# Performance work log

Measured on AMD Instinct MI355X. Metric: run time of the kernel, lower is better.

Reference implementation:

```python
import jax, jax.numpy as jnp
import numpy as np
import math

B, DG, P, DA = 512, 1024, 1024, 256
LN_EPS = 1e-5  # torch LayerNorm default
EPS = 1e-12


def _ln(x, g, b):
    mu = jnp.mean(x, axis=-1, keepdims=True)
    var = jnp.mean((x - mu) ** 2, axis=-1, keepdims=True)
    return (x - mu) * jax.lax.rsqrt(var + LN_EPS) * g + b


def setup_inputs() -> dict:
    key = jax.random.key(0)
    ks = jax.random.split(key, 16)
    s = lambda fan_in: 1.0 / math.sqrt(fan_in)
    return {
        "hg": jax.random.normal(ks[0], (B, DG), jnp.float32),
        "desc_2d": jax.random.normal(ks[1], (B, P), jnp.float32),
        "Wq": jax.random.uniform(ks[2], (DA, DG), jnp.float32, -s(DG), s(DG)),
        "bq": jnp.zeros((DA,), jnp.float32),
        "wk_val": jax.random.uniform(ks[3], (DA,), jnp.float32, -1.0, 1.0),
        "bk_val": jax.random.uniform(ks[4], (DA,), jnp.float32, -1.0, 1.0),
        "wv_val": jax.random.uniform(ks[5], (DA,), jnp.float32, -1.0, 1.0),
        "bv_val": jax.random.uniform(ks[6], (DA,), jnp.float32, -1.0, 1.0),
        "Ek": jax.random.normal(ks[7], (P, DA), jnp.float32),
        "Ev": jax.random.normal(ks[8], (P, DA), jnp.float32),
        "Uq": jax.random.uniform(ks[9], (DA, DA), jnp.float32, -s(DA), s(DA)),
        "Vk": jax.random.uniform(ks[10], (DA, DA), jnp.float32, -s(DA), s(DA)),
        "ln_q_g": jnp.ones((DA,), jnp.float32), "ln_q_b": jnp.zeros((DA,), jnp.float32),
        "ln_k_g": jnp.ones((DA,), jnp.float32), "ln_k_b": jnp.zeros((DA,), jnp.float32),
        "ln_v_g": jnp.ones((DA,), jnp.float32), "ln_v_b": jnp.zeros((DA,), jnp.float32),
    }


def reference(hg, desc_2d, Wq, bq, wk_val, bk_val, wv_val, bv_val, Ek, Ev, Uq, Vk,
              ln_q_g, ln_q_b, ln_k_g, ln_k_b, ln_v_g, ln_v_b):
    # dropout is inference-mode (identity)
    q = _ln(hg @ Wq.T + bq, ln_q_g, ln_q_b)                       # (B, DA)
    # scalar -> token proj plus id embedding
    k = desc_2d[:, :, None] * wk_val + bk_val + Ek[None]          # (B, P, DA)
    v = desc_2d[:, :, None] * wv_val + bv_val + Ev[None]
    k = _ln(k, ln_k_g, ln_k_b)
    v = _ln(v, ln_v_g, ln_v_b)
    q2 = q @ Uq.T                                                 # (B, DA)
    k2 = jnp.einsum('bpd,ed->bpe', k, Vk)                         # (B, P, DA)
    e = jnp.einsum('bpd,bd->bp', k2, q2) / math.sqrt(DA)          # (B, P)
    alpha = jax.nn.sigmoid(e)
    alpha = alpha / (jnp.sum(alpha, axis=1, keepdims=True) + EPS)
    c = jnp.einsum('bp,bpd->bd', alpha, v)                        # (B, DA)
    return c, alpha
```

## Files before the change

### kernel.cpp

```cpp
#include <hip/hip_runtime.h>
#include <math.h>

#define B 512
#define DG 1024
#define P 1024
#define DA 256
#define LDP 68

__device__ __forceinline__ float block_reduce_sum(float v, volatile float* red) {
    #pragma unroll
    for (int off = 32; off > 0; off >>= 1) v += __shfl_down(v, off, 64);
    const int lane = threadIdx.x & 63, wid = threadIdx.x >> 6;
    __syncthreads();
    if (lane == 0) red[wid] = v;
    __syncthreads();
    return red[0] + red[1] + red[2] + red[3];
}

#define FMA16(a4, b4, acc)                                   \
    acc[0][0] = fmaf(a4.x, b4.x, acc[0][0]);                 \
    acc[0][1] = fmaf(a4.x, b4.y, acc[0][1]);                 \
    acc[0][2] = fmaf(a4.x, b4.z, acc[0][2]);                 \
    acc[0][3] = fmaf(a4.x, b4.w, acc[0][3]);                 \
    acc[1][0] = fmaf(a4.y, b4.x, acc[1][0]);                 \
    acc[1][1] = fmaf(a4.y, b4.y, acc[1][1]);                 \
    acc[1][2] = fmaf(a4.y, b4.z, acc[1][2]);                 \
    acc[1][3] = fmaf(a4.y, b4.w, acc[1][3]);                 \
    acc[2][0] = fmaf(a4.z, b4.x, acc[2][0]);                 \
    acc[2][1] = fmaf(a4.z, b4.y, acc[2][1]);                 \
    acc[2][2] = fmaf(a4.z, b4.z, acc[2][2]);                 \
    acc[2][3] = fmaf(a4.z, b4.w, acc[2][3]);                 \
    acc[3][0] = fmaf(a4.w, b4.x, acc[3][0]);                 \
    acc[3][1] = fmaf(a4.w, b4.y, acc[3][1]);                 \
    acc[3][2] = fmaf(a4.w, b4.z, acc[3][2]);                 \
    acc[3][3] = fmaf(a4.w, b4.w, acc[3][3]);

#define FMA8(a0, a1, b4, acc)                                \
    acc[0][0] = fmaf(a0, b4.x, acc[0][0]);                   \
    acc[0][1] = fmaf(a0, b4.y, acc[0][1]);                   \
    acc[0][2] = fmaf(a0, b4.z, acc[0][2]);                   \
    acc[0][3] = fmaf(a0, b4.w, acc[0][3]);                   \
    acc[1][0] = fmaf(a1, b4.x, acc[1][0]);                   \
    acc[1][1] = fmaf(a1, b4.y, acc[1][1]);                   \
    acc[1][2] = fmaf(a1, b4.z, acc[1][2]);                   \
    acc[1][3] = fmaf(a1, b4.w, acc[1][3]);

__global__ __launch_bounds__(256) void KA(const float* __restrict__ hg, const float* __restrict__ Wq,
                                          const float* __restrict__ Uq, const float* __restrict__ Vk,
                                          const float* __restrict__ Ek, const float* __restrict__ Ev,
                                          const float* __restrict__ wk, const float* __restrict__ bk,
                                          const float* __restrict__ wv, const float* __restrict__ bv,
                                          const float* __restrict__ gk, const float* __restrict__ bkln,
                                          float* __restrict__ qp, float* __restrict__ Gm,
                                          float* __restrict__ pst, float* __restrict__ scal4,
                                          float* __restrict__ vec4) {
    __shared__ __align__(16) float sA[32 * LDP];
    __shared__ __align__(16) float sB[32 * LDP];
    __shared__ float red[4];
    const int tid = threadIdx.x;
    const int bi = blockIdx.x;

    if (bi < 256) {
        const int mt = bi & 7, nt = (bi >> 3) & 3, ks = bi >> 5;
        const int b0 = mt * 64, d0 = nt * 64, kc = ks * 128;
        const int sm = tid >> 3, sk4 = (tid & 7) * 4;
        const int ty4 = (tid >> 4) * 4, tx4 = (tid & 15) * 4;
        float acc[4][4] = {};
        for (int kt = 0; kt < 128; kt += 32) {
            const int kg = kc + kt;
            #pragma unroll
            for (int pass = 0; pass < 2; ++pass) {
                int m = sm + pass * 32;
                float4 av = *reinterpret_cast<const float4*>(&hg[(b0 + m) * DG + kg + sk4]);
                sA[(sk4 + 0) * LDP + m] = av.x; sA[(sk4 + 1) * LDP + m] = av.y;
                sA[(sk4 + 2) * LDP + m] = av.z; sA[(sk4 + 3) * LDP + m] = av.w;
                float4 wv4 = *reinterpret_cast<const float4*>(&Wq[(d0 + m) * DG + kg + sk4]);
                sB[(sk4 + 0) * LDP + m] = wv4.x; sB[(sk4 + 1) * LDP + m] = wv4.y;
                sB[(sk4 + 2) * LDP + m] = wv4.z; sB[(sk4 + 3) * LDP + m] = wv4.w;
            }
            __syncthreads();
            #pragma unroll
            for (int kk = 0; kk < 32; ++kk) {
                float4 a4 = *reinterpret_cast<const float4*>(&sA[kk * LDP + ty4]);
                float4 b4 = *reinterpret_cast<const float4*>(&sB[kk * LDP + tx4]);
                FMA16(a4, b4, acc)
            }
            __syncthreads();
        }
        float* outp = qp + ks * (B * DA);
        #pragma unroll
        for (int i = 0; i < 4; ++i) {
            float4 o = make_float4(acc[i][0], acc[i][1], acc[i][2], acc[i][3]);
            *reinterpret_cast<float4*>(&outp[(b0 + ty4 + i) * DA + d0 + tx4]) = o;
        }
    } else if (bi < 384) {
        const int b2 = bi - 256;
        const int e0 = (b2 & 7) * 32, p0 = (b2 >> 3) * 64;
        const int sm = tid >> 3, sk4 = (tid & 7) * 4;
        const int ty = tid >> 4, tx4 = (tid & 15) * 4;
        float acc[2][4] = {};
        for (int kt = 0; kt < 256; kt += 32) {
            float4 vv = *reinterpret_cast<const float4*>(&Vk[(e0 + sm) * DA + kt + sk4]);
            float4 gg = *reinterpret_cast<const float4*>(&gk[kt + sk4]);
            sA[(sk4 + 0) * LDP + sm] = vv.x * gg.x; sA[(sk4 + 1) * LDP + sm] = vv.y * gg.y;
            sA[(sk4 + 2) * LDP + sm] = vv.z * gg.z; sA[(sk4 + 3) * LDP + sm] = vv.w * gg.w;
            #pragma unroll
            for (int pass = 0; pass < 2; ++pass) {
                int m = sm + pass * 32;
                float4 ee = *reinterpret_cast<const float4*>(&Ek[(p0 + m) * DA + kt + sk4]);
                sB[(sk4 + 0) * LDP + m] = ee.x; sB[(sk4 + 1) * LDP + m] = ee.y;
                sB[(sk4 + 2) * LDP + m] = ee.z; sB[(sk4 + 3) * LDP + m] = ee.w;
            }
            __syncthreads();
            #pragma unroll
            for (int kk = 0; kk < 32; ++kk) {
                float a0 = sA[kk * LDP + ty * 2 + 0];
                float a1 = sA[kk * LDP + ty * 2 + 1];
                float4 b4 = *reinterpret_cast<const float4*>(&sB[kk * LDP + tx4]);
                FMA8(a0, a1, b4, acc)
            }
            __syncthreads();
        }
        #pragma unroll
        for (int i = 0; i < 2; ++i) {
            float4 o = make_float4(acc[i][0], acc[i][1], acc[i][2], acc[i][3]);
            *reinterpret_cast<float4*>(&Gm[(e0 + ty * 2 + i) * P + p0 + tx4]) = o;
        }
    } else if (bi == 384) {
        float* w4  = sA;
        float* tmp = sB;
        float gkd = gk[tid];
        w4[0 * 256 + tid] = wk[tid] * gkd;
        w4[1 * 256 + tid] = bk[tid] * gkd;
        w4[2 * 256 + tid] = gkd;
        w4[3 * 256 + tid] = bkln[tid];
        __syncthreads();
        const int dl = tid & 15, eg = tid >> 4;
        for (int eb = 0; eb < 16; ++eb) {
            int e = eb * 16 + eg;
            float p0 = 0.f, p1 = 0.f, p2 = 0.f, p3 = 0.f;
            #pragma unroll
            for (int t = 0; t < 16; ++t) {
                int d = dl + t * 16;
                float v = Vk[e * DA + d];
                p0 = fmaf(v, w4[d], p0);
                p1 = fmaf(v, w4[256 + d], p1);
                p2 = fmaf(v, w4[512 + d], p2);
                p3 = fmaf(v, w4[768 + d], p3);
            }
            #pragma unroll
            for (int m = 8; m > 0; m >>= 1) {
                p0 += __shfl_xor(p0, m, 16);
                p1 += __shfl_xor(p1, m, 16);
                p2 += __shfl_xor(p2, m, 16);
                p3 += __shfl_xor(p3, m, 16);
            }
            if (dl == 0) {
                tmp[e * 4 + 0] = p0; tmp[e * 4 + 1] = p1;
                tmp[e * 4 + 2] = p2; tmp[e * 4 + 3] = p3;
            }
        }
        __syncthreads();
        float a0 = 0.f, a1 = 0.f, a2 = 0.f, a3 = 0.f;
        for (int e = 0; e < 256; ++e) {
            float u = Uq[e * DA + tid];
            a0 = fmaf(u, tmp[e * 4 + 0], a0);
            a1 = fmaf(u, tmp[e * 4 + 1], a1);
            a2 = fmaf(u, tmp[e * 4 + 2], a2);
            a3 = fmaf(u, tmp[e * 4 + 3], a3);
        }
        vec4[tid] = a0; vec4[256 + tid] = a1; vec4[512 + tid] = a2; vec4[768 + tid] = a3;
    } else {
        const int p = bi - 385, d = tid;
        const float inv = 1.0f / DA;
        float ek = Ek[p * DA + d], ev = Ev[p * DA + d];
        float wkd = wk[d], wvd = wv[d];
        float ck = bk[d] + ek, cv = bv[d] + ev;

        float Sck  = block_reduce_sum(ck, red);
        float Sck2 = block_reduce_sum(ck * ck, red);
        float Swck = block_reduce_sum(wkd * ck, red);
        float Scv  = block_reduce_sum(cv, red);
        float Scv2 = block_reduce_sum(cv * cv, red);
        float Swcv = block_reduce_sum(wvd * cv, red);
        float Swk  = block_reduce_sum(wkd, red);
        float Swv  = block_reduce_sum(wvd, red);

        float mwk = Swk * inv, mwv = Swv * inv;
        float mck = Sck * inv, mcv = Scv * inv;
        if (d == 0) {
            pst[0 * P + p] = mck;
            pst[1 * P + p] = Swck * inv - mwk * mck;
            pst[2 * P + p] = Sck2 * inv - mck * mck;
            pst[3 * P + p] = mcv;
            pst[4 * P + p] = Swcv * inv - mwv * mcv;
            pst[5 * P + p] = Scv2 * inv - mcv * mcv;
        }
        if (p == 0) {
            float Swk2 = block_reduce_sum(wkd * wkd, red);
            float Swv2 = block_reduce_sum(wvd * wvd, red);
            if (d == 0) {
                scal4[0] = mwk;
                scal4[1] = Swk2 * inv - mwk * mwk;
                scal4[2] = mwv;
                scal4[3] = Swv2 * inv - mwv * mwv;
            }
        }
    }
}

__global__ __launch_bounds__(256) void KC(const float* __restrict__ qp, const float* __restrict__ bq,
                                          const float* __restrict__ gq, const float* __restrict__ bqln,
                                          const float* __restrict__ vec4, const float* __restrict__ Uq,
                                          const float* __restrict__ Gm,
                                          float* __restrict__ qout, float* __restrict__ Nm,
                                          float* __restrict__ bscal) {
    __shared__ __align__(16) float sA[32 * LDP];
    __shared__ __align__(16) float sB[32 * LDP];
    __shared__ float red[4];
    const int tid = threadIdx.x;
    const int bi = blockIdx.x;

    if (bi < 512) {
        const int b = bi, d = tid;
        float x = bq[d];
        #pragma unroll
        for (int ks = 0; ks < 8; ++ks) x += qp[ks * (B * DA) + b * DA + d];
        float mu = block_reduce_sum(x, red) * (1.0f / DA);
        float xc = x - mu;
        float var = block_reduce_sum(xc * xc, red) * (1.0f / DA);
        float qv = xc * rsqrtf(var + 1e-5f) * gq[d] + bqln[d];
        qout[b * DA + d] = qv;
        float Wg = block_reduce_sum(qv * vec4[d], red);
        float Cg = block_reduce_sum(qv * vec4[256 + d], red);
        float G_ = block_reduce_sum(qv * vec4[512 + d], red);
        float Bb = block_reduce_sum(qv * vec4[768 + d], red);
        if (d == 0) {
            bscal[b] = Wg; bscal[B + b] = Cg; bscal[2 * B + b] = G_; bscal[3 * B + b] = Bb;
        }
    } else {
        const int b2 = bi - 512;
        const int f0 = (b2 & 7) * 32, p0 = (b2 >> 3) * 64;
        const int sm = tid >> 3, sk4 = (tid & 7) * 4;
        const int kr = tid >> 4, n4 = (tid & 15) * 4;
        const int ty = tid >> 4, tx4 = (tid & 15) * 4;
        float acc[2][4] = {};
        for (int kt = 0; kt < 256; kt += 32) {
            *reinterpret_cast<float4*>(&sA[sm * LDP + sk4]) =
                *reinterpret_cast<const float4*>(&Uq[(kt + sm) * DA + f0 + sk4]);
            #pragma unroll
            for (int pass = 0; pass < 2; ++pass) {
                int k = kr + pass * 16;
                *reinterpret_cast<float4*>(&sB[k * LDP + n4]) =
                    *reinterpret_cast<const float4*>(&Gm[(kt + k) * P + p0 + n4]);
            }
            __syncthreads();
            #pragma unroll
            for (int kk = 0; kk < 32; ++kk) {
                float a0 = sA[kk * LDP + ty * 2 + 0];
                float a1 = sA[kk * LDP + ty * 2 + 1];
                float4 b4 = *reinterpret_cast<const float4*>(&sB[kk * LDP + tx4]);
                FMA8(a0, a1, b4, acc)
            }
            __syncthreads();
        }
        #pragma unroll
        for (int i = 0; i < 2; ++i) {
            float4 o = make_float4(acc[i][0], acc[i][1], acc[i][2], acc[i][3]);
            *reinterpret_cast<float4*>(&Nm[(f0 + ty * 2 + i) * P + p0 + tx4]) = o;
        }
    }
}

__global__ __launch_bounds__(256) void KD(const float* __restrict__ q, const float* __restrict__ Nm,
                                          const float* __restrict__ desc, const float* __restrict__ bscal,
                                          const float* __restrict__ pst, const float* __restrict__ scal4,
                                          float* __restrict__ u_out, float* __restrict__ w) {
    __shared__ __align__(16) float sA[32 * LDP];
    __shared__ __align__(16) float sB[32 * LDP];
    const int tid = threadIdx.x, bi = blockIdx.x;
    const int b0 = (bi & 15) * 32, p0 = (bi >> 4) * 64;
    const int sm = tid >> 3, sk4 = (tid & 7) * 4;
    const int kr = tid >> 4, n4 = (tid & 15) * 4;
    const int ty = tid >> 4, tx4 = (tid & 15) * 4;
    float acc[2][4] = {};
    for (int kt = 0; kt < 256; kt += 32) {
        float4 qv4 = *reinterpret_cast<const float4*>(&q[(b0 + sm) * DA + kt + sk4]);
        sA[(sk4 + 0) * LDP + sm] = qv4.x; sA[(sk4 + 1) * LDP + sm] = qv4.y;
        sA[(sk4 + 2) * LDP + sm] = qv4.z; sA[(sk4 + 3) * LDP + sm] = qv4.w;
        #pragma unroll
        for (int pass = 0; pass < 2; ++pass) {
            int k = kr + pass * 16;
            *reinterpret_cast<float4*>(&sB[k * LDP + n4]) =
                *reinterpret_cast<const float4*>(&Nm[(kt + k) * P + p0 + n4]);
        }
        __syncthreads();
        #pragma unroll
        for (int kk = 0; kk < 32; ++kk) {
            float a0 = sA[kk * LDP + ty * 2 + 0];
            float a1 = sA[kk * LDP + ty * 2 + 1];
            float4 b4 = *reinterpret_cast<const float4*>(&sB[kk * LDP + tx4]);
            FMA8(a0, a1, b4, acc)
        }
        __syncthreads();
    }
    const float mwk = scal4[0], Ak = scal4[1], Av = scal4[3];
    #pragma unroll
    for (int i = 0; i < 2; ++i) {
        int b = b0 + ty * 2 + i;
        float Wg = bscal[b], Cg = bscal[B + b], G_ = bscal[2 * B + b], Bb = bscal[3 * B + b];
        float4 uo, wo;
        float* up = &uo.x; float* wp = &wo.x;
        #pragma unroll
        for (int j = 0; j < 4; ++j) {
            int p = p0 + tx4 + j;
            float s = desc[b * P + p];
            float mck = pst[p], Bk = pst[P + p], Ck = pst[2 * P + p];
            float var = fmaf(s, fmaf(s, Ak, 2.0f * Bk), Ck);
            float rstd = rsqrtf(var + 1e-5f);
            float mu = fmaf(s, mwk, mck);
            float e = (rstd * (fmaf(s, Wg, Cg) + acc[i][j] - mu * G_) + Bb) * 0.0625f;
            float uu = 1.0f / (1.0f + expf(-e));
            float Bv = pst[4 * P + p], Cv = pst[5 * P + p];
            float varv = fmaf(s, fmaf(s, Av, 2.0f * Bv), Cv);
            float rv = rsqrtf(varv + 1e-5f);
            up[j] = uu; wp[j] = uu * rv;
        }
        *reinterpret_cast<float4*>(&u_out[b * P + p0 + tx4]) = uo;
        *reinterpret_cast<float4*>(&w[b * P + p0 + tx4]) = wo;
    }
}

__global__ __launch_bounds__(256) void KF(const float* __restrict__ w, const float* __restrict__ Ev,
                                          float* __restrict__ cpart) {
    __shared__ __align__(16) float sA[32 * LDP];
    __shared__ __align__(16) float sB[32 * LDP];
    const int tid = threadIdx.x, bi = blockIdx.x;
    const int mt = bi & 7, nt = (bi >> 3) & 3, ks = bi >> 5;
    const int b0 = mt * 64, d0 = nt * 64, kc = ks * 64;
    const int sm = tid >> 3, sk4 = (tid & 7) * 4;
    const int kr = tid >> 4, n4 = (tid & 15) * 4;
    const int ty4 = (tid >> 4) * 4, tx4 = (tid & 15) * 4;
    float acc[4][4] = {};
    for (int kt = 0; kt < 64; kt += 32) {
        const int kg = kc + kt;
        #pragma unroll
        for (int pass = 0; pass < 2; ++pass) {
            int m = sm + pass * 32;
            float4 av = *reinterpret_cast<const float4*>(&w[(b0 + m) * P + kg + sk4]);
            sA[(sk4 + 0) * LDP + m] = av.x; sA[(sk4 + 1) * LDP + m] = av.y;
            sA[(sk4 + 2) * LDP + m] = av.z; sA[(sk4 + 3) * LDP + m] = av.w;
            int k = kr + pass * 16;
            *reinterpret_cast<float4*>(&sB[k * LDP + n4]) =
                *reinterpret_cast<const float4*>(&Ev[(kg + k) * DA + d0 + n4]);
        }
        __syncthreads();
        #pragma unroll
        for (int kk = 0; kk < 32; ++kk) {
            float4 a4 = *reinterpret_cast<const float4*>(&sA[kk * LDP + ty4]);
            float4 b4 = *reinterpret_cast<const float4*>(&sB[kk * LDP + tx4]);
            FMA16(a4, b4, acc)
        }
        __syncthreads();
    }
    float* outp = cpart + ks * (B * DA);
    #pragma unroll
    for (int i = 0; i < 4; ++i) {
        float4 o = make_float4(acc[i][0], acc[i][1], acc[i][2], acc[i][3]);
        *reinterpret_cast<float4*>(&outp[(b0 + ty4 + i) * DA + d0 + tx4]) = o;
    }
}

__global__ __launch_bounds__(256) void KG(const float* __restrict__ desc, const float* __restrict__ pst,
                                          const float* __restrict__ scal4, const float* __restrict__ cpart,
                                          const float* __restrict__ gv, const float* __restrict__ wv,
                                          const float* __restrict__ bvv, const float* __restrict__ bvln,
                                          float* __restrict__ alpha_io, const float* __restrict__ wbuf,
                                          float* __restrict__ out_c) {
    __shared__ float red[4];
    const int b = blockIdx.x, tid = threadIdx.x;
    const float mwv = scal4[2];
    float u[4], wl[4], sv[4], mv[4];
    #pragma unroll
    for (int j = 0; j < 4; ++j) {
        int p = j * 256 + tid;
        u[j]  = alpha_io[b * P + p];
        wl[j] = wbuf[b * P + p];
        sv[j] = desc[b * P + p];
        mv[j] = fmaf(sv[j], mwv, pst[3 * P + p]);
    }
    float S   = block_reduce_sum(u[0] + u[1] + u[2] + u[3], red);
    float SB  = block_reduce_sum(wl[0] + wl[1] + wl[2] + wl[3], red);
    float SBs = block_reduce_sum(wl[0]*sv[0] + wl[1]*sv[1] + wl[2]*sv[2] + wl[3]*sv[3], red);
    float SBm = block_reduce_sum(wl[0]*mv[0] + wl[1]*mv[1] + wl[2]*mv[2] + wl[3]*mv[3], red);
    float invS = 1.0f / (S + 1e-12f);
    float T = S * invS;
    #pragma unroll
    for (int j = 0; j < 4; ++j)
        alpha_io[b * P + j * 256 + tid] = u[j] * invS;
    const int d = tid;
    float csum = 0.f;
    #pragma unroll
    for (int ks = 0; ks < 16; ++ks) csum += cpart[ks * (B * DA) + b * DA + d];
    out_c[b * DA + d] = invS * (gv[d] * (wv[d] * SBs + bvv[d] * SB + csum - SBm)) + bvln[d] * T;
}

extern "C" void kernel_launch(void* const* d_in, const int* in_sizes, int n_in,
                              void* d_out, int out_size, void* d_ws, size_t ws_size,
                              hipStream_t stream) {
    (void)in_sizes; (void)n_in; (void)out_size; (void)ws_size;
    const float* hg   = (const float*)d_in[0];
    const float* desc = (const float*)d_in[1];
    const float* Wq   = (const float*)d_in[2];
    const float* bq   = (const float*)d_in[3];
    const float* wk   = (const float*)d_in[4];
    const float* bk   = (const float*)d_in[5];
    const float* wv   = (const float*)d_in[6];
    const float* bv   = (const float*)d_in[7];
    const float* Ek   = (const float*)d_in[8];
    const float* Ev   = (const float*)d_in[9];
    const float* Uq   = (const float*)d_in[10];
    const float* Vk   = (const float*)d_in[11];
    const float* gq   = (const float*)d_in[12];
    const float* bqln = (const float*)d_in[13];
    const float* gk   = (const float*)d_in[14];
    const float* bkln = (const float*)d_in[15];
    const float* gv   = (const float*)d_in[16];
    const float* bvln = (const float*)d_in[17];

    float* out = (float*)d_out;
    float* out_c = out;
    float* out_alpha = out + B * DA;

    float* ws = (float*)d_ws;
    float* qp    = ws;
    float* Gm    = ws + 1048576;
    float* Nm    = ws + 1310720;
    float* q     = ws + 1572864;
    float* w     = ws + 1703936;
    float* cpart = ws + 2228224;
    float* vec4  = ws + 4325376;
    float* bscal = ws + 4326400;
    float* pst   = ws + 4328448;
    float* scal4 = ws + 4334592;

    KA<<<1409, 256, 0, stream>>>(hg, Wq, Uq, Vk, Ek, Ev, wk, bk, wv, bv, gk, bkln,
                                 qp, Gm, pst, scal4, vec4);
    KC<<<640, 256, 0, stream>>>(qp, bq, gq, bqln, vec4, Uq, Gm, q, Nm, bscal);
    KD<<<256, 256, 0, stream>>>(q, Nm, desc, bscal, pst, scal4, out_alpha, w);
    KF<<<512, 256, 0, stream>>>(w, Ev, cpart);
    KG<<<512, 256, 0, stream>>>(desc, pst, scal4, cpart, gv, wv, bv, bvln, out_alpha, w, out_c);
}
```

Before: 66.47 us.

## Reassociate Uq·Vk product, split-K score GEMM, fold c-reduction into atomic epilogue

Restructures the attention pipeline. It precomputes H = Uq^T·(gk∘Vk) as a small split-K GEMM instead of forming Gm = Vk·Ek^T, then computes N from H and Ek. The per-batch scores come from a split-K q·N GEMM followed by a fused sigmoid/normalization kernel. The final Ev GEMM now scales by invS·gv and atomically adds into out_c, which removes the 16-way cpart buffer and its reduction pass. Per-position LN statistics use wave-level shuffle reductions over four positions per block instead of block reductions. In exchange it adds more partial-sum buffers, float atomics (non-deterministic summation order), and relies on the output being written before KF runs.

```diff
diff --git a/kernel.cpp b/kernel.cpp
--- a/kernel.cpp
+++ b/kernel.cpp
@@ -6,6 +6,8 @@
 #define P 1024
 #define DA 256
 #define LDP 68
+#define BP (B * P)
+#define BD (B * DA)
 
 __device__ __forceinline__ float block_reduce_sum(float v, volatile float* red) {
     #pragma unroll
@@ -15,6 +17,12 @@
     if (lane == 0) red[wid] = v;
     __syncthreads();
     return red[0] + red[1] + red[2] + red[3];
+}
+
+__device__ __forceinline__ float wsum(float v) {
+    #pragma unroll
+    for (int m = 32; m > 0; m >>= 1) v += __shfl_xor(v, m, 64);
+    return v;
 }
 
 #define FMA16(a4, b4, acc)                                   \
@@ -35,15 +43,69 @@
     acc[3][2] = fmaf(a4.w, b4.z, acc[3][2]);                 \
     acc[3][3] = fmaf(a4.w, b4.w, acc[3][3]);
 
-#define FMA8(a0, a1, b4, acc)                                \
-    acc[0][0] = fmaf(a0, b4.x, acc[0][0]);                   \
-    acc[0][1] = fmaf(a0, b4.y, acc[0][1]);                   \
-    acc[0][2] = fmaf(a0, b4.z, acc[0][2]);                   \
-    acc[0][3] = fmaf(a0, b4.w, acc[0][3]);                   \
-    acc[1][0] = fmaf(a1, b4.x, acc[1][0]);                   \
-    acc[1][1] = fmaf(a1, b4.y, acc[1][1]);                   \
-    acc[1][2] = fmaf(a1, b4.z, acc[1][2]);                   \
-    acc[1][3] = fmaf(a1, b4.w, acc[1][3]);
+__device__ __forceinline__ void stage_T(const float* __restrict__ src, int ldk, int m0, int k0,
+                                        int tid, float* sD) {
+    const int m = tid >> 3, k4 = (tid & 7) * 4;
+    #pragma unroll
+    for (int pass = 0; pass < 2; ++pass) {
+        int mm = m + pass * 32;
+        float4 v = *reinterpret_cast<const float4*>(&src[(m0 + mm) * ldk + k0 + k4]);
+        sD[(k4 + 0) * LDP + mm] = v.x; sD[(k4 + 1) * LDP + mm] = v.y;
+        sD[(k4 + 2) * LDP + mm] = v.z; sD[(k4 + 3) * LDP + mm] = v.w;
+    }
+}
+__device__ __forceinline__ void stage_T4(const float* __restrict__ src, int pstride, int ldk,
+                                         int m0, int k0, int tid, float* sD) {
+    const int m = tid >> 3, k4 = (tid & 7) * 4;
+    #pragma unroll
+    for (int pass = 0; pass < 2; ++pass) {
+        int mm = m + pass * 32;
+        const float* base = &src[(m0 + mm) * ldk + k0 + k4];
+        float4 v = *reinterpret_cast<const float4*>(base);
+        #pragma unroll
+        for (int s = 1; s < 4; ++s) {
+            float4 w = *reinterpret_cast<const float4*>(base + s * pstride);
+            v.x += w.x; v.y += w.y; v.z += w.z; v.w += w.w;
+        }
+        sD[(k4 + 0) * LDP + mm] = v.x; sD[(k4 + 1) * LDP + mm] = v.y;
+        sD[(k4 + 2) * LDP + mm] = v.z; sD[(k4 + 3) * LDP + mm] = v.w;
+    }
+}
+__device__ __forceinline__ void stage_N1(const float* __restrict__ src, int ldn, int k0, int n0,
+                                         int tid, float* sD) {
+    const int k = tid >> 4, n4 = (tid & 15) * 4;
+    #pragma unroll
+    for (int pass = 0; pass < 2; ++pass) {
+        int kk = k + pass * 16;
+        *reinterpret_cast<float4*>(&sD[kk * LDP + n4]) =
+            *reinterpret_cast<const float4*>(&src[(k0 + kk) * ldn + n0 + n4]);
+    }
+}
+__device__ __forceinline__ void stage_N4(const float* __restrict__ src, int pstride, int ldn,
+                                         int k0, int n0, int tid, float* sD) {
+    const int k = tid >> 4, n4 = (tid & 15) * 4;
+    #pragma unroll
+    for (int pass = 0; pass < 2; ++pass) {
+        int kk = k + pass * 16;
+        const float* base = &src[(k0 + kk) * ldn + n0 + n4];
+        float4 v = *reinterpret_cast<const float4*>(base);
+        #pragma unroll
+        for (int s = 1; s < 4; ++s) {
+            float4 w = *reinterpret_cast<const float4*>(base + s * pstride);
+            v.x += w.x; v.y += w.y; v.z += w.z; v.w += w.w;
+        }
+        *reinterpret_cast<float4*>(&sD[kk * LDP + n4]) = v;
+    }
+}
+__device__ __forceinline__ void mm_inner(const float* sA, const float* sB, int tid, float acc[4][4]) {
+    const int ty4 = (tid >> 4) * 4, tx4 = (tid & 15) * 4;
+    #pragma unroll
+    for (int kk = 0; kk < 32; ++kk) {
+        float4 a4 = *reinterpret_cast<const float4*>(&sA[kk * LDP + ty4]);
+        float4 b4 = *reinterpret_cast<const float4*>(&sB[kk * LDP + tx4]);
+        FMA16(a4, b4, acc)
+    }
+}
 
 __global__ __launch_bounds__(256) void KA(const float* __restrict__ hg, const float* __restrict__ Wq,
                                           const float* __restrict__ Uq, const float* __restrict__ Vk,
@@ -51,82 +113,61 @@
                                           const float* __restrict__ wk, const float* __restrict__ bk,
                                           const float* __restrict__ wv, const float* __restrict__ bv,
                                           const float* __restrict__ gk, const float* __restrict__ bkln,
-                                          float* __restrict__ qp, float* __restrict__ Gm,
+                                          float* __restrict__ qp, float* __restrict__ Hp,
                                           float* __restrict__ pst, float* __restrict__ scal4,
                                           float* __restrict__ vec4) {
     __shared__ __align__(16) float sA[32 * LDP];
     __shared__ __align__(16) float sB[32 * LDP];
-    __shared__ float red[4];
     const int tid = threadIdx.x;
-    const int bi = blockIdx.x;
-
-    if (bi < 256) {
-        const int mt = bi & 7, nt = (bi >> 3) & 3, ks = bi >> 5;
-        const int b0 = mt * 64, d0 = nt * 64, kc = ks * 128;
-        const int sm = tid >> 3, sk4 = (tid & 7) * 4;
-        const int ty4 = (tid >> 4) * 4, tx4 = (tid & 15) * 4;
+    const int t = blockIdx.x;
+    const int ty4 = (tid >> 4) * 4, tx4 = (tid & 15) * 4;
+
+    if (t < 512) {
+        const int mt = t & 7, nt = (t >> 3) & 3, ks = t >> 5;
+        const int b0 = mt * 64, d0 = nt * 64, kc = ks * 64;
         float acc[4][4] = {};
-        for (int kt = 0; kt < 128; kt += 32) {
-            const int kg = kc + kt;
-            #pragma unroll
-            for (int pass = 0; pass < 2; ++pass) {
-                int m = sm + pass * 32;
-                float4 av = *reinterpret_cast<const float4*>(&hg[(b0 + m) * DG + kg + sk4]);
-                sA[(sk4 + 0) * LDP + m] = av.x; sA[(sk4 + 1) * LDP + m] = av.y;
-                sA[(sk4 + 2) * LDP + m] = av.z; sA[(sk4 + 3) * LDP + m] = av.w;
-                float4 wv4 = *reinterpret_cast<const float4*>(&Wq[(d0 + m) * DG + kg + sk4]);
-                sB[(sk4 + 0) * LDP + m] = wv4.x; sB[(sk4 + 1) * LDP + m] = wv4.y;
-                sB[(sk4 + 2) * LDP + m] = wv4.z; sB[(sk4 + 3) * LDP + m] = wv4.w;
-            }
-            __syncthreads();
-            #pragma unroll
-            for (int kk = 0; kk < 32; ++kk) {
-                float4 a4 = *reinterpret_cast<const float4*>(&sA[kk * LDP + ty4]);
-                float4 b4 = *reinterpret_cast<const float4*>(&sB[kk * LDP + tx4]);
-                FMA16(a4, b4, acc)
-            }
-            __syncthreads();
-        }
-        float* outp = qp + ks * (B * DA);
+        for (int kt = 0; kt < 64; kt += 32) {
+            stage_T(hg, DG, b0, kc + kt, tid, sA);
+            stage_T(Wq, DG, d0, kc + kt, tid, sB);
+            __syncthreads();
+            mm_inner(sA, sB, tid, acc);
+            __syncthreads();
+        }
+        float* outp = qp + ks * BD;
         #pragma unroll
         for (int i = 0; i < 4; ++i) {
             float4 o = make_float4(acc[i][0], acc[i][1], acc[i][2], acc[i][3]);
             *reinterpret_cast<float4*>(&outp[(b0 + ty4 + i) * DA + d0 + tx4]) = o;
         }
-    } else if (bi < 384) {
-        const int b2 = bi - 256;
-        const int e0 = (b2 & 7) * 32, p0 = (b2 >> 3) * 64;
-        const int sm = tid >> 3, sk4 = (tid & 7) * 4;
-        const int ty = tid >> 4, tx4 = (tid & 15) * 4;
-        float acc[2][4] = {};
-        for (int kt = 0; kt < 256; kt += 32) {
-            float4 vv = *reinterpret_cast<const float4*>(&Vk[(e0 + sm) * DA + kt + sk4]);
-            float4 gg = *reinterpret_cast<const float4*>(&gk[kt + sk4]);
-            sA[(sk4 + 0) * LDP + sm] = vv.x * gg.x; sA[(sk4 + 1) * LDP + sm] = vv.y * gg.y;
-            sA[(sk4 + 2) * LDP + sm] = vv.z * gg.z; sA[(sk4 + 3) * LDP + sm] = vv.w * gg.w;
-            #pragma unroll
-            for (int pass = 0; pass < 2; ++pass) {
-                int m = sm + pass * 32;
-                float4 ee = *reinterpret_cast<const float4*>(&Ek[(p0 + m) * DA + kt + sk4]);
-                sB[(sk4 + 0) * LDP + m] = ee.x; sB[(sk4 + 1) * LDP + m] = ee.y;
-                sB[(sk4 + 2) * LDP + m] = ee.z; sB[(sk4 + 3) * LDP + m] = ee.w;
+    } else if (t < 576) {
+        const int t2 = t - 512;
+        const int ft = t2 & 3, dt = (t2 >> 2) & 3, ks = t2 >> 4;
+        const int f0 = ft * 64, d0 = dt * 64, kc = ks * 64;
+        float acc[4][4] = {};
+        for (int kt = 0; kt < 64; kt += 32) {
+            stage_N1(Uq, DA, kc + kt, f0, tid, sA);
+            {
+                const int k = tid >> 4, n4 = (tid & 15) * 4;
+                float4 g = *reinterpret_cast<const float4*>(&gk[d0 + n4]);
+                #pragma unroll
+                for (int pass = 0; pass < 2; ++pass) {
+                    int kk = k + pass * 16;
+                    float4 v = *reinterpret_cast<const float4*>(&Vk[(kc + kt + kk) * DA + d0 + n4]);
+                    v.x *= g.x; v.y *= g.y; v.z *= g.z; v.w *= g.w;
+                    *reinterpret_cast<float4*>(&sB[kk * LDP + n4]) = v;
+                }
             }
             __syncthreads();
-            #pragma unroll
-            for (int kk = 0; kk < 32; ++kk) {
-                float a0 = sA[kk * LDP + ty * 2 + 0];
-                float a1 = sA[kk * LDP + ty * 2 + 1];
-                float4 b4 = *reinterpret_cast<const float4*>(&sB[kk * LDP + tx4]);
-                FMA8(a0, a1, b4, acc)
-            }
-            __syncthreads();
-        }
-        #pragma unroll
-        for (int i = 0; i < 2; ++i) {
+            mm_inner(sA, sB, tid, acc);
+            __syncthreads();
+        }
+        float* outp = Hp + ks * (DA * DA);
+        #pragma unroll
+        for (int i = 0; i < 4; ++i) {
             float4 o = make_float4(acc[i][0], acc[i][1], acc[i][2], acc[i][3]);
-            *reinterpret_cast<float4*>(&Gm[(e0 + ty * 2 + i) * P + p0 + tx4]) = o;
-        }
-    } else if (bi == 384) {
+            *reinterpret_cast<float4*>(&outp[(f0 + ty4 + i) * DA + d0 + tx4]) = o;
+        }
+    } else if (t == 576) {
         float* w4  = sA;
         float* tmp = sB;
         float gkd = gk[tid];
@@ -140,8 +181,8 @@
             int e = eb * 16 + eg;
             float p0 = 0.f, p1 = 0.f, p2 = 0.f, p3 = 0.f;
             #pragma unroll
-            for (int t = 0; t < 16; ++t) {
-                int d = dl + t * 16;
+            for (int tt = 0; tt < 16; ++tt) {
+                int d = dl + tt * 16;
                 float v = Vk[e * DA + d];
                 p0 = fmaf(v, w4[d], p0);
                 p1 = fmaf(v, w4[256 + d], p1);
@@ -171,24 +212,30 @@
         }
         vec4[tid] = a0; vec4[256 + tid] = a1; vec4[512 + tid] = a2; vec4[768 + tid] = a3;
     } else {
-        const int p = bi - 385, d = tid;
+        const int tp = t - 577;
+        const int wid = tid >> 6, lane = tid & 63;
+        const int p = tp * 4 + wid;
+        const int d4 = lane * 4;
         const float inv = 1.0f / DA;
-        float ek = Ek[p * DA + d], ev = Ev[p * DA + d];
-        float wkd = wk[d], wvd = wv[d];
-        float ck = bk[d] + ek, cv = bv[d] + ev;
-
-        float Sck  = block_reduce_sum(ck, red);
-        float Sck2 = block_reduce_sum(ck * ck, red);
-        float Swck = block_reduce_sum(wkd * ck, red);
-        float Scv  = block_reduce_sum(cv, red);
-        float Scv2 = block_reduce_sum(cv * cv, red);
-        float Swcv = block_reduce_sum(wvd * cv, red);
-        float Swk  = block_reduce_sum(wkd, red);
-        float Swv  = block_reduce_sum(wvd, red);
-
+        float4 ek4 = *reinterpret_cast<const float4*>(&Ek[p * DA + d4]);
+        float4 ev4 = *reinterpret_cast<const float4*>(&Ev[p * DA + d4]);
+        float4 wk4 = *reinterpret_cast<const float4*>(&wk[d4]);
+        float4 bk4 = *reinterpret_cast<const float4*>(&bk[d4]);
+        float4 wv4 = *reinterpret_cast<const float4*>(&wv[d4]);
+        float4 bv4 = *reinterpret_cast<const float4*>(&bv[d4]);
+        float ck0 = bk4.x + ek4.x, ck1 = bk4.y + ek4.y, ck2 = bk4.z + ek4.z, ck3 = bk4.w + ek4.w;
+        float cv0 = bv4.x + ev4.x, cv1 = bv4.y + ev4.y, cv2 = bv4.z + ev4.z, cv3 = bv4.w + ev4.w;
+        float Sck  = wsum(ck0 + ck1 + ck2 + ck3);
+        float Sck2 = wsum(ck0*ck0 + ck1*ck1 + ck2*ck2 + ck3*ck3);
+        float Swck = wsum(wk4.x*ck0 + wk4.y*ck1 + wk4.z*ck2 + wk4.w*ck3);
+        float Scv  = wsum(cv0 + cv1 + cv2 + cv3);
+        float Scv2 = wsum(cv0*cv0 + cv1*cv1 + cv2*cv2 + cv3*cv3);
+        float Swcv = wsum(wv4.x*cv0 + wv4.y*cv1 + wv4.z*cv2 + wv4.w*cv3);
+        float Swk  = wsum(wk4.x + wk4.y + wk4.z + wk4.w);
+        float Swv  = wsum(wv4.x + wv4.y + wv4.z + wv4.w);
         float mwk = Swk * inv, mwv = Swv * inv;
         float mck = Sck * inv, mcv = Scv * inv;
-        if (d == 0) {
+        if (lane == 0) {
             pst[0 * P + p] = mck;
             pst[1 * P + p] = Swck * inv - mwk * mck;
             pst[2 * P + p] = Sck2 * inv - mck * mck;
@@ -197,9 +244,9 @@
             pst[5 * P + p] = Scv2 * inv - mcv * mcv;
         }
         if (p == 0) {
-            float Swk2 = block_reduce_sum(wkd * wkd, red);
-            float Swv2 = block_reduce_sum(wvd * wvd, red);
-            if (d == 0) {
+            float Swk2 = wsum(wk4.x*wk4.x + wk4.y*wk4.y + wk4.z*wk4.z + wk4.w*wk4.w);
+            float Swv2 = wsum(wv4.x*wv4.x + wv4.y*wv4.y + wv4.z*wv4.z + wv4.w*wv4.w);
+            if (lane == 0) {
                 scal4[0] = mwk;
                 scal4[1] = Swk2 * inv - mwk * mwk;
                 scal4[2] = mwv;
@@ -211,21 +258,21 @@
 
 __global__ __launch_bounds__(256) void KC(const float* __restrict__ qp, const float* __restrict__ bq,
                                           const float* __restrict__ gq, const float* __restrict__ bqln,
-                                          const float* __restrict__ vec4, const float* __restrict__ Uq,
-                                          const float* __restrict__ Gm,
-                                          float* __restrict__ qout, float* __restrict__ Nm,
+                                          const float* __restrict__ vec4, const float* __restrict__ Hp,
+                                          const float* __restrict__ Ek,
+                                          float* __restrict__ qout, float* __restrict__ Np,
                                           float* __restrict__ bscal) {
     __shared__ __align__(16) float sA[32 * LDP];
     __shared__ __align__(16) float sB[32 * LDP];
     __shared__ float red[4];
     const int tid = threadIdx.x;
-    const int bi = blockIdx.x;
-
-    if (bi < 512) {
-        const int b = bi, d = tid;
+    const int t = blockIdx.x;
+
+    if (t < 512) {
+        const int b = t, d = tid;
         float x = bq[d];
         #pragma unroll
-        for (int ks = 0; ks < 8; ++ks) x += qp[ks * (B * DA) + b * DA + d];
+        for (int ks = 0; ks < 16; ++ks) x += qp[ks * BD + b * DA + d];
         float mu = block_reduce_sum(x, red) * (1.0f / DA);
         float xc = x - mu;
         float var = block_reduce_sum(xc * xc, red) * (1.0f / DA);
@@ -236,173 +283,132 @@
         float G_ = block_reduce_sum(qv * vec4[512 + d], red);
         float Bb = block_reduce_sum(qv * vec4[768 + d], red);
         if (d == 0) {
-            bscal[b] = Wg; bscal[B + b] = Cg; bscal[2 * B + b] = G_; bscal[3 * B + b] = Bb;
+            bscal[b] = Wg; bscal[B + b] = Cg;
+            bscal[2 * B + b] = G_; bscal[3 * B + b] = Bb;
         }
     } else {
-        const int b2 = bi - 512;
-        const int f0 = (b2 & 7) * 32, p0 = (b2 >> 3) * 64;
-        const int sm = tid >> 3, sk4 = (tid & 7) * 4;
-        const int kr = tid >> 4, n4 = (tid & 15) * 4;
-        const int ty = tid >> 4, tx4 = (tid & 15) * 4;
-        float acc[2][4] = {};
-        for (int kt = 0; kt < 256; kt += 32) {
-            *reinterpret_cast<float4*>(&sA[sm * LDP + sk4]) =
-                *reinterpret_cast<const float4*>(&Uq[(kt + sm) * DA + f0 + sk4]);
-            #pragma unroll
-            for (int pass = 0; pass < 2; ++pass) {
-                int k = kr + pass * 16;
-                *reinterpret_cast<float4*>(&sB[k * LDP + n4]) =
-                    *reinterpret_cast<const float4*>(&Gm[(kt + k) * P + p0 + n4]);
-            }
-            __syncthreads();
-            #pragma unroll
-            for (int kk = 0; kk < 32; ++kk) {
-                float a0 = sA[kk * LDP + ty * 2 + 0];
-                float a1 = sA[kk * LDP + ty * 2 + 1];
-                float4 b4 = *reinterpret_cast<const float4*>(&sB[kk * LDP + tx4]);
-                FMA8(a0, a1, b4, acc)
-            }
-            __syncthreads();
-        }
-        #pragma unroll
-        for (int i = 0; i < 2; ++i) {
+        const int ty4 = (tid >> 4) * 4, tx4 = (tid & 15) * 4;
+        const int t2 = t - 512;
+        const int ft = t2 & 3, pt = (t2 >> 2) & 15, ks = t2 >> 6;
+        const int f0 = ft * 64, p0 = pt * 64, kc = ks * 64;
+        float acc[4][4] = {};
+        for (int kt = 0; kt < 64; kt += 32) {
+            stage_T4(Hp, DA * DA, DA, f0, kc + kt, tid, sA);
+            stage_T(Ek, DA, p0, kc + kt, tid, sB);
+            __syncthreads();
+            mm_inner(sA, sB, tid, acc);
+            __syncthreads();
+        }
+        float* outp = Np + ks * (DA * P);
+        #pragma unroll
+        for (int i = 0; i < 4; ++i) {
             float4 o = make_float4(acc[i][0], acc[i][1], acc[i][2], acc[i][3]);
-            *reinterpret_cast<float4*>(&Nm[(f0 + ty * 2 + i) * P + p0 + tx4]) = o;
-        }
-    }
-}
-
-__global__ __launch_bounds__(256) void KD(const float* __restrict__ q, const float* __restrict__ Nm,
-                                          const float* __restrict__ desc, const float* __restrict__ bscal,
-                                          const float* __restrict__ pst, const float* __restrict__ scal4,
-                                          float* __restrict__ u_out, float* __restrict__ w) {
+            *reinterpret_cast<float4*>(&outp[(f0 + ty4 + i) * P + p0 + tx4]) = o;
+        }
+    }
+}
+
+__global__ __launch_bounds__(256) void KD(const float* __restrict__ q, const float* __restrict__ Np,
+                                          float* __restrict__ epart) {
     __shared__ __align__(16) float sA[32 * LDP];
     __shared__ __align__(16) float sB[32 * LDP];
-    const int tid = threadIdx.x, bi = blockIdx.x;
-    const int b0 = (bi & 15) * 32, p0 = (bi >> 4) * 64;
-    const int sm = tid >> 3, sk4 = (tid & 7) * 4;
-    const int kr = tid >> 4, n4 = (tid & 15) * 4;
-    const int ty = tid >> 4, tx4 = (tid & 15) * 4;
-    float acc[2][4] = {};
-    for (int kt = 0; kt < 256; kt += 32) {
-        float4 qv4 = *reinterpret_cast<const float4*>(&q[(b0 + sm) * DA + kt + sk4]);
-        sA[(sk4 + 0) * LDP + sm] = qv4.x; sA[(sk4 + 1) * LDP + sm] = qv4.y;
-        sA[(sk4 + 2) * LDP + sm] = qv4.z; sA[(sk4 + 3) * LDP + sm] = qv4.w;
-        #pragma unroll
-        for (int pass = 0; pass < 2; ++pass) {
-            int k = kr + pass * 16;
-            *reinterpret_cast<float4*>(&sB[k * LDP + n4]) =
-                *reinterpret_cast<const float4*>(&Nm[(kt + k) * P + p0 + n4]);
-        }
-        __syncthreads();
-        #pragma unroll
-        for (int kk = 0; kk < 32; ++kk) {
-            float a0 = sA[kk * LDP + ty * 2 + 0];
-            float a1 = sA[kk * LDP + ty * 2 + 1];
-            float4 b4 = *reinterpret_cast<const float4*>(&sB[kk * LDP + tx4]);
-            FMA8(a0, a1, b4, acc)
-        }
-        __syncthreads();
-    }
-    const float mwk = scal4[0], Ak = scal4[1], Av = scal4[3];
-    #pragma unroll
-    for (int i = 0; i < 2; ++i) {
-        int b = b0 + ty * 2 + i;
-        float Wg = bscal[b], Cg = bscal[B + b], G_ = bscal[2 * B + b], Bb = bscal[3 * B + b];
-        float4 uo, wo;
-        float* up = &uo.x; float* wp = &wo.x;
-        #pragma unroll
-        for (int j = 0; j < 4; ++j) {
-            int p = p0 + tx4 + j;
-            float s = desc[b * P + p];
-            float mck = pst[p], Bk = pst[P + p], Ck = pst[2 * P + p];
-            float var = fmaf(s, fmaf(s, Ak, 2.0f * Bk), Ck);
-            float rstd = rsqrtf(var + 1e-5f);
-            float mu = fmaf(s, mwk, mck);
-            float e = (rstd * (fmaf(s, Wg, Cg) + acc[i][j] - mu * G_) + Bb) * 0.0625f;
-            float uu = 1.0f / (1.0f + expf(-e));
-            float Bv = pst[4 * P + p], Cv = pst[5 * P + p];
-            float varv = fmaf(s, fmaf(s, Av, 2.0f * Bv), Cv);
-            float rv = rsqrtf(varv + 1e-5f);
-            up[j] = uu; wp[j] = uu * rv;
-        }
-        *reinterpret_cast<float4*>(&u_out[b * P + p0 + tx4]) = uo;
-        *reinterpret_cast<float4*>(&w[b * P + p0 + tx4]) = wo;
-    }
-}
-
-__global__ __launch_bounds__(256) void KF(const float* __restrict__ w, const float* __restrict__ Ev,
-                                          float* __restrict__ cpart) {
+    const int tid = threadIdx.x, t = blockIdx.x;
+    const int ty4 = (tid >> 4) * 4, tx4 = (tid & 15) * 4;
+    const int bt = t & 7, pt = (t >> 3) & 15, ks = t >> 7;
+    const int b0 = bt * 64, p0 = pt * 64, kc = ks * 64;
+    float acc[4][4] = {};
+    for (int kt = 0; kt < 64; kt += 32) {
+        stage_T(q, DA, b0, kc + kt, tid, sA);
+        stage_N4(Np, DA * P, P, kc + kt, p0, tid, sB);
+        __syncthreads();
+        mm_inner(sA, sB, tid, acc);
+        __syncthreads();
+    }
+    float* outp = epart + ks * BP;
+    #pragma unroll
+    for (int i = 0; i < 4; ++i) {
+        float4 o = make_float4(acc[i][0], acc[i][1], acc[i][2], acc[i][3]);
+        *reinterpret_cast<float4*>(&outp[(b0 + ty4 + i) * P + p0 + tx4]) = o;
+    }
+}
+
+__global__ __launch_bounds__(256) void KE(const float* __restrict__ epart, const float* __restrict__ desc,
+                                          const float* __restrict__ bscal, const float* __restrict__ pst,
+                                          const float* __restrict__ scal4,
+                                          const float* __restrict__ gv, const float* __restrict__ wv,
+                                          const float* __restrict__ bvv, const float* __restrict__ bvln,
+                                          float* __restrict__ alpha_out, float* __restrict__ wbuf,
+                                          float* __restrict__ bscal2, float* __restrict__ out_c) {
+    __shared__ float red[4];
+    const int b = blockIdx.x, tid = threadIdx.x;
+    const float mwk = scal4[0], Ak = scal4[1], mwv = scal4[2], Av = scal4[3];
+    const float Wg = bscal[b], Cg = bscal[B + b], G_ = bscal[2 * B + b], Bb = bscal[3 * B + b];
+    float u[4];
+    float us = 0.f, ws_ = 0.f, wss = 0.f, wms = 0.f;
+    #pragma unroll
+    for (int j = 0; j < 4; ++j) {
+        int p = j * 256 + tid;
+        float dot = epart[b * P + p] + epart[BP + b * P + p]
+                  + epart[2 * BP + b * P + p] + epart[3 * BP + b * P + p];
+        float s = desc[b * P + p];
+        float mck = pst[p], Bk = pst[P + p], Ck = pst[2 * P + p];
+        float var = fmaf(s, fmaf(s, Ak, 2.0f * Bk), Ck);
+        float rstd = rsqrtf(var + 1e-5f);
+        float mu = fmaf(s, mwk, mck);
+        float e = (rstd * (fmaf(s, Wg, Cg) + dot - mu * G_) + Bb) * 0.0625f;
+        float uu = 1.0f / (1.0f + expf(-e));
+        float mcv = pst[3 * P + p], Bv = pst[4 * P + p], Cv = pst[5 * P + p];
+        float varv = fmaf(s, fmaf(s, Av, 2.0f * Bv), Cv);
+        float rv = rsqrtf(varv + 1e-5f);
+        float ww = uu * rv;
+        wbuf[b * P + p] = ww;
+        u[j] = uu;
+        us += uu; ws_ += ww;
+        wss = fmaf(ww, s, wss);
+        wms = fmaf(ww, fmaf(s, mwv, mcv), wms);
+    }
+    float S   = block_reduce_sum(us, red);
+    float SB  = block_reduce_sum(ws_, red);
+    float SBs = block_reduce_sum(wss, red);
+    float SBm = block_reduce_sum(wms, red);
+    float invS = 1.0f / (S + 1e-12f);
+    float T = S * invS;
+    #pragma unroll
+    for (int j = 0; j < 4; ++j)
+        alpha_out[b * P + j * 256 + tid] = u[j] * invS;
+    if (tid == 0) bscal2[b] = invS;
+    const int d = tid;
+    out_c[b * DA + d] = invS * (gv[d] * (wv[d] * SBs + bvv[d] * SB - SBm)) + bvln[d] * T;
+}
+
+__global__ __launch_bounds__(256) void KF(const float* __restrict__ wbuf, const float* __restrict__ Ev,
+                                          const float* __restrict__ bscal2, const float* __restrict__ gv,
+                                          float* __restrict__ out_c) {
     __shared__ __align__(16) float sA[32 * LDP];
     __shared__ __align__(16) float sB[32 * LDP];
-    const int tid = threadIdx.x, bi = blockIdx.x;
-    const int mt = bi & 7, nt = (bi >> 3) & 3, ks = bi >> 5;
+    const int tid = threadIdx.x, t = blockIdx.x;
+    const int ty4 = (tid >> 4) * 4, tx4 = (tid & 15) * 4;
+    const int mt = t & 7, nt = (t >> 3) & 3, ks = t >> 5;
     const int b0 = mt * 64, d0 = nt * 64, kc = ks * 64;
-    const int sm = tid >> 3, sk4 = (tid & 7) * 4;
-    const int kr = tid >> 4, n4 = (tid & 15) * 4;
-    const int ty4 = (tid >> 4) * 4, tx4 = (tid & 15) * 4;
     float acc[4][4] = {};
     for (int kt = 0; kt < 64; kt += 32) {
-        const int kg = kc + kt;
-        #pragma unroll
-        for (int pass = 0; pass < 2; ++pass) {
-            int m = sm + pass * 32;
-            float4 av = *reinterpret_cast<const float4*>(&w[(b0 + m) * P + kg + sk4]);
-            sA[(sk4 + 0) * LDP + m] = av.x; sA[(sk4 + 1) * LDP + m] = av.y;
-            sA[(sk4 + 2) * LDP + m] = av.z; sA[(sk4 + 3) * LDP + m] = av.w;
-            int k = kr + pass * 16;
-            *reinterpret_cast<float4*>(&sB[k * LDP + n4]) =
-                *reinterpret_cast<const float4*>(&Ev[(kg + k) * DA + d0 + n4]);
-        }
-        __syncthreads();
-        #pragma unroll
-        for (int kk = 0; kk < 32; ++kk) {
-            float4 a4 = *reinterpret_cast<const float4*>(&sA[kk * LDP + ty4]);
-            float4 b4 = *reinterpret_cast<const float4*>(&sB[kk * LDP + tx4]);
-            FMA16(a4, b4, acc)
-        }
-        __syncthreads();
-    }
-    float* outp = cpart + ks * (B * DA);
+        stage_T(wbuf, P, b0, kc + kt, tid, sA);
+        stage_N1(Ev, DA, kc + kt, d0, tid, sB);
+        __syncthreads();
+        mm_inner(sA, sB, tid, acc);
+        __syncthreads();
+    }
+    float4 g4 = *reinterpret_cast<const float4*>(&gv[d0 + tx4]);
     #pragma unroll
     for (int i = 0; i < 4; ++i) {
-        float4 o = make_float4(acc[i][0], acc[i][1], acc[i][2], acc[i][3]);
-        *reinterpret_cast<float4*>(&outp[(b0 + ty4 + i) * DA + d0 + tx4]) = o;
-    }
-}
-
-__global__ __launch_bounds__(256) void KG(const float* __restrict__ desc, const float* __restrict__ pst,
-                                          const float* __restrict__ scal4, const float* __restrict__ cpart,
-                                          const float* __restrict__ gv, const float* __restrict__ wv,
-                                          const float* __restrict__ bvv, const float* __restrict__ bvln,
-                                          float* __restrict__ alpha_io, const float* __restrict__ wbuf,
-                                          float* __restrict__ out_c) {
-    __shared__ float red[4];
-    const int b = blockIdx.x, tid = threadIdx.x;
-    const float mwv = scal4[2];
-    float u[4], wl[4], sv[4], mv[4];
-    #pragma unroll
-    for (int j = 0; j < 4; ++j) {
-        int p = j * 256 + tid;
-        u[j]  = alpha_io[b * P + p];
-        wl[j] = wbuf[b * P + p];
-        sv[j] = desc[b * P + p];
-        mv[j] = fmaf(sv[j], mwv, pst[3 * P + p]);
-    }
-    float S   = block_reduce_sum(u[0] + u[1] + u[2] + u[3], red);
-    float SB  = block_reduce_sum(wl[0] + wl[1] + wl[2] + wl[3], red);
-    float SBs = block_reduce_sum(wl[0]*sv[0] + wl[1]*sv[1] + wl[2]*sv[2] + wl[3]*sv[3], red);
-    float SBm = block_reduce_sum(wl[0]*mv[0] + wl[1]*mv[1] + wl[2]*mv[2] + wl[3]*mv[3], red);
-    float invS = 1.0f / (S + 1e-12f);
-    float T = S * invS;
-    #pragma unroll
-    for (int j = 0; j < 4; ++j)
-        alpha_io[b * P + j * 256 + tid] = u[j] * invS;
-    const int d = tid;
-    float csum = 0.f;
-    #pragma unroll
-    for (int ks = 0; ks < 16; ++ks) csum += cpart[ks * (B * DA) + b * DA + d];
-    out_c[b * DA + d] = invS * (gv[d] * (wv[d] * SBs + bvv[d] * SB + csum - SBm)) + bvln[d] * T;
+        const int b = b0 + ty4 + i;
+        const float sc = bscal2[b];
+        float* dst = &out_c[b * DA + d0 + tx4];
+        atomicAdd(dst + 0, acc[i][0] * sc * g4.x);
+        atomicAdd(dst + 1, acc[i][1] * sc * g4.y);
+        atomicAdd(dst + 2, acc[i][2] * sc * g4.z);
+        atomicAdd(dst + 3, acc[i][3] * sc * g4.w);
+    }
 }
 
 extern "C" void kernel_launch(void* const* d_in, const int* in_sizes, int n_in,
@@ -430,24 +436,26 @@
 
     float* out = (float*)d_out;
     float* out_c = out;
-    float* out_alpha = out + B * DA;
+    float* out_alpha = out + BD;
 
     float* ws = (float*)d_ws;
     float* qp    = ws;
-    float* Gm    = ws + 1048576;
-    float* Nm    = ws + 1310720;
-    float* q     = ws + 1572864;
-    float* w     = ws + 1703936;
-    float* cpart = ws + 2228224;
-    float* vec4  = ws + 4325376;
-    float* bscal = ws + 4326400;
-    float* pst   = ws + 4328448;
-    float* scal4 = ws + 4334592;
-
-    KA<<<1409, 256, 0, stream>>>(hg, Wq, Uq, Vk, Ek, Ev, wk, bk, wv, bv, gk, bkln,
-                                 qp, Gm, pst, scal4, vec4);
-    KC<<<640, 256, 0, stream>>>(qp, bq, gq, bqln, vec4, Uq, Gm, q, Nm, bscal);
-    KD<<<256, 256, 0, stream>>>(q, Nm, desc, bscal, pst, scal4, out_alpha, w);
-    KF<<<512, 256, 0, stream>>>(w, Ev, cpart);
-    KG<<<512, 256, 0, stream>>>(desc, pst, scal4, cpart, gv, wv, bv, bvln, out_alpha, w, out_c);
-}
+    float* Hp    = ws + 2097152;
+    float* Np    = ws + 2359296;
+    float* q     = ws + 3407872;
+    float* epart = ws + 3538944;
+    float* wbuf  = ws + 5636096;
+    float* vec4  = ws + 6160384;
+    float* bscal = ws + 6161408;
+    float* bscal2= ws + 6163456;
+    float* pst   = ws + 6163968;
+    float* scal4 = ws + 6170112;
+
+    KA<<<833, 256, 0, stream>>>(hg, Wq, Uq, Vk, Ek, Ev, wk, bk, wv, bv, gk, bkln,
+                                qp, Hp, pst, scal4, vec4);
+    KC<<<768, 256, 0, stream>>>(qp, bq, gq, bqln, vec4, Hp, Ek, q, Np, bscal);
+    KD<<<512, 256, 0, stream>>>(q, Np, epart);
+    KE<<<512, 256, 0, stream>>>(epart, desc, bscal, pst, scal4, gv, wv, bv, bvln,
+                                out_alpha, wbuf, bscal2, out_c);
+    KF<<<512, 256, 0, stream>>>(wbuf, Ev, bscal2, gv, out_c);
+}
```

After: 85.88 us. 29.2% more time.
